# Performance work log

Measured on AMD Instinct MI355X. Metric: run time of the kernel, lower is better.

The kernel has to match this reference:

```python
import jax, jax.numpy as jnp
import numpy as np

NUM_USERS = 100000
NUM_ITEMS = 200000
N_NODES = NUM_USERS + NUM_ITEMS
LATENT_DIM = 64
N_LAYERS = 3
NNZ = 4000000


def setup_inputs() -> dict:
    key = jax.random.key(0)
    k1, k2, k3, k4, k5 = jax.random.split(key, 5)
    user_emb = 0.1 * jax.random.normal(k1, (NUM_USERS, LATENT_DIM), dtype=jnp.float32)
    item_emb = 0.1 * jax.random.normal(k2, (NUM_ITEMS, LATENT_DIM), dtype=jnp.float32)
    edge_rows = jax.random.randint(k3, (NNZ,), 0, N_NODES, dtype=jnp.int32)
    edge_cols = jax.random.randint(k4, (NNZ,), 0, N_NODES, dtype=jnp.int32)
    # normalized adjacency values (positive, small, like 1/sqrt(d_i d_j))
    edge_vals = jax.random.uniform(k5, (NNZ,), dtype=jnp.float32) * 0.1
    return {"user_emb": user_emb, "item_emb": item_emb,
            "edge_rows": edge_rows, "edge_cols": edge_cols, "edge_vals": edge_vals}


def _spmm(edge_rows, edge_cols, edge_vals, x, n):
    # sparse (COO) @ dense: gather source rows, scale, scatter-add to dest rows
    msg = edge_vals[:, None] * x[edge_cols]          # [nnz, D]
    return jax.ops.segment_sum(msg, edge_rows, num_segments=n)


def reference(user_emb, item_emb, edge_rows, edge_cols, edge_vals):
    n_users = user_emb.shape[0]
    n = n_users + item_emb.shape[0]
    all_emb = jnp.concatenate([user_emb, item_emb], axis=0)  # [N, D]
    embs = [all_emb]
    for _ in range(N_LAYERS):
        all_emb = _spmm(edge_rows, edge_cols, edge_vals, all_emb, n)
        embs.append(all_emb)
    light_out = jnp.mean(jnp.stack(embs, axis=1), axis=1)   # [N, D]
    users = light_out[:n_users]
    items = light_out[n_users:]
    return users, items
```

## Files before the change

kernel.cpp:

```cpp
#include <hip/hip_runtime.h>


#define N_USERS  100000
#define N_ITEMS  200000
#define N_NODES_ 300000
#define DIM      64
#define NNZ_     4000000
#define BSHIFT   10
#define NBUCKET  ((N_NODES_ + 1023) >> 10)
#define BCAP     14336
#define PA_CHUNK 4096
#define PA_BLOCKS ((NNZ_ + PA_CHUNK - 1) / PA_CHUNK)

typedef float        f32x4 __attribute__((ext_vector_type(4)));
typedef unsigned int u32x4 __attribute__((ext_vector_type(4)));
typedef int          i32x2 __attribute__((ext_vector_type(2)));
__device__ __forceinline__ float4 ntload_f4(const float4* p) {
    f32x4 v = __builtin_nontemporal_load((const f32x4*)p);
    return make_float4(v.x, v.y, v.z, v.w);
}
__device__ __forceinline__ uint4 ntload_u4(const uint4* p) {
    u32x4 v = __builtin_nontemporal_load((const u32x4*)p);
    return make_uint4(v.x, v.y, v.z, v.w);
}
__device__ __forceinline__ void ntstore_f4(float4* p, float4 x) {
    f32x4 v = {x.x, x.y, x.z, x.w};
    __builtin_nontemporal_store(v, (f32x4*)p);
}
__device__ __forceinline__ int2 ntload_i2(const int2* p) {
    i32x2 v = __builtin_nontemporal_load((const i32x2*)p);
    return make_int2(v.x, v.y);
}

__device__ __forceinline__ unsigned short f2bf(float f) {
    unsigned u = __float_as_uint(f);
    unsigned r = 0x7fffu + ((u >> 16) & 1u);
    return (unsigned short)((u + r) >> 16);
}
__device__ __forceinline__ void fma8(float* acc, float v, uint4 r) {
    acc[0] = fmaf(v, __uint_as_float(r.x << 16), acc[0]);
    acc[1] = fmaf(v, __uint_as_float(r.x & 0xffff0000u), acc[1]);
    acc[2] = fmaf(v, __uint_as_float(r.y << 16), acc[2]);
    acc[3] = fmaf(v, __uint_as_float(r.y & 0xffff0000u), acc[3]);
    acc[4] = fmaf(v, __uint_as_float(r.z << 16), acc[4]);
    acc[5] = fmaf(v, __uint_as_float(r.z & 0xffff0000u), acc[5]);
    acc[6] = fmaf(v, __uint_as_float(r.w << 16), acc[6]);
    acc[7] = fmaf(v, __uint_as_float(r.w & 0xffff0000u), acc[7]);
}
__device__ __forceinline__ uint4 pack8(const float* f) {
    unsigned a = (unsigned)f2bf(f[0]) | ((unsigned)f2bf(f[1]) << 16);
    unsigned b = (unsigned)f2bf(f[2]) | ((unsigned)f2bf(f[3]) << 16);
    unsigned c = (unsigned)f2bf(f[4]) | ((unsigned)f2bf(f[5]) << 16);
    unsigned d = (unsigned)f2bf(f[6]) | ((unsigned)f2bf(f[7]) << 16);
    return make_uint4(a, b, c, d);
}
__device__ __forceinline__ void unpack8(float* f, uint4 r) {
    f[0] = __uint_as_float(r.x << 16); f[1] = __uint_as_float(r.x & 0xffff0000u);
    f[2] = __uint_as_float(r.y << 16); f[3] = __uint_as_float(r.y & 0xffff0000u);
    f[4] = __uint_as_float(r.z << 16); f[5] = __uint_as_float(r.z & 0xffff0000u);
    f[6] = __uint_as_float(r.w << 16); f[7] = __uint_as_float(r.w & 0xffff0000u);
}

__global__ void init_bf(const float4* __restrict__ u, const float4* __restrict__ it,
                        uint4* __restrict__ Abf) {
    const int n_u = N_USERS * DIM / 8;
    const int n_t = N_NODES_ * DIM / 8;
    int i = blockIdx.x * blockDim.x + threadIdx.x;
    if (i >= n_t) return;
    float4 a, b;
    if (i < n_u) { a = u[2 * i];           b = u[2 * i + 1]; }
    else         { int j = i - n_u; a = it[2 * j]; b = it[2 * j + 1]; }
    float f[8] = {a.x, a.y, a.z, a.w, b.x, b.y, b.z, b.w};
    Abf[i] = pack8(f);
}

__global__ void gcur_init2(int* __restrict__ gcursor) {
    int t = threadIdx.x;
    if (t < NBUCKET) gcursor[t] = t * BCAP;
}

__global__ __launch_bounds__(256) void passA(const int* __restrict__ rows,
                                             const int* __restrict__ cols,
                                             const float* __restrict__ vals,
                                             int* __restrict__ gcursor,
                                             int2* __restrict__ binned) {
    __shared__ int  hist[NBUCKET];
    __shared__ int  base_l[NBUCKET];
    __shared__ int  gshift[NBUCKET];
    __shared__ int  sc[256];
    __shared__ int2 stage[PA_CHUNK];
    __shared__ unsigned short bIdA[PA_CHUNK];

    int tid = threadIdx.x;
    int base = blockIdx.x * PA_CHUNK;
    int cnt = NNZ_ - base; if (cnt > PA_CHUNK) cnt = PA_CHUNK;

    for (int i = tid; i < NBUCKET; i += 256) hist[i] = 0;
    __syncthreads();

    int rr[16], cc[16], vv[16];
    #pragma unroll
    for (int k = 0; k < 16; ++k) {
        int i = tid + (k << 8);
        if (i < cnt) {
            int e = base + i;
            rr[k] = rows[e];
            cc[k] = cols[e];
            vv[k] = __float_as_int(vals[e]);
            atomicAdd(&hist[rr[k] >> BSHIFT], 1);
        } else rr[k] = -1;
    }
    __syncthreads();

    int i0 = 2 * tid, i1 = 2 * tid + 1;
    int c0 = (i0 < NBUCKET) ? hist[i0] : 0;
    int c1 = (i1 < NBUCKET) ? hist[i1] : 0;
    sc[tid] = c0 + c1;
    __syncthreads();
    for (int off = 1; off < 256; off <<= 1) {
        int t = (tid >= off) ? sc[tid - off] : 0;
        __syncthreads();
        sc[tid] += t;
        __syncthreads();
    }
    int excl = (tid == 0) ? 0 : sc[tid - 1];
    if (i0 < NBUCKET) {
        base_l[i0] = excl;
        int g0 = c0 ? atomicAdd(&gcursor[i0], c0) : 0;
        gshift[i0] = g0 - excl;
        hist[i0] = 0;
    }
    if (i1 < NBUCKET) {
        base_l[i1] = excl + c0;
        int g1 = c1 ? atomicAdd(&gcursor[i1], c1) : 0;
        gshift[i1] = g1 - (excl + c0);
        hist[i1] = 0;
    }
    __syncthreads();

    #pragma unroll
    for (int k = 0; k < 16; ++k) {
        if (rr[k] >= 0) {
            int b = rr[k] >> BSHIFT;
            int kk = atomicAdd(&hist[b], 1);
            int pos = base_l[b] + kk;
            stage[pos] = make_int2(cc[k] | ((rr[k] & 1023) << 19), vv[k]);
            bIdA[pos] = (unsigned short)b;
        }
    }
    __syncthreads();

    #pragma unroll
    for (int k = 0; k < 16; ++k) {
        int i = tid + (k << 8);
        if (i < cnt) binned[gshift[bIdA[i]] + i] = stage[i];
    }
}

__global__ void bucket_scan(const int* __restrict__ gcursor,
                            int* __restrict__ bucket_base,
                            int* __restrict__ row_start) {
    __shared__ int lds[512];
    int t = threadIdx.x;
    int c = (t < NBUCKET) ? (gcursor[t] - t * BCAP) : 0;
    lds[t] = c;
    __syncthreads();
    for (int off = 1; off < 512; off <<= 1) {
        int v = (t >= off) ? lds[t - off] : 0;
        __syncthreads();
        lds[t] += v;
        __syncthreads();
    }
    if (t < NBUCKET) bucket_base[t] = lds[t] - c;
    if (t == 0) row_start[N_NODES_] = NNZ_;
}

__global__ __launch_bounds__(1024) void passB(const int* __restrict__ gcursor,
                                              const int* __restrict__ bucket_base,
                                              const int2* __restrict__ binned,
                                              int* __restrict__ row_start,
                                              int2* __restrict__ sedge) {
    __shared__ int lcnt[1024];
    __shared__ int wsum[16];
    int b = blockIdx.x;
    int t = threadIdx.x;
    int base = b * BCAP;
    int cnt = gcursor[b] - base;
    int csr0 = bucket_base[b];
    lcnt[t] = 0;
    __syncthreads();

    int lo[14], hv[14];
    #pragma unroll
    for (int k = 0; k < 14; ++k) {
        int i = t + (k << 10);
        if (i < cnt) {
            int2 p = ntload_i2(&binned[base + i]);
            lo[k] = p.x; hv[k] = p.y;
            atomicAdd(&lcnt[((unsigned)p.x >> 19) & 1023], 1);
        } else lo[k] = -1;
    }
    __syncthreads();

    int v = lcnt[t];
    int lane = t & 63;
    int wid = t >> 6;
    int sv = v;
    #pragma unroll
    for (int off = 1; off < 64; off <<= 1) {
        int tmp = __shfl_up(sv, off);
        if (lane >= off) sv += tmp;
    }
    if (lane == 63) wsum[wid] = sv;
    __syncthreads();
    if (t < 16) {
        int ws = wsum[t];
        #pragma unroll
        for (int off = 1; off < 16; off <<= 1) {
            int tmp = __shfl_up(ws, off);
            if (t >= off) ws += tmp;
        }
        wsum[t] = ws;
    }
    __syncthreads();
    int wbase = (wid == 0) ? 0 : wsum[wid - 1];
    int excl = wbase + sv - v;

    int gr = (b << BSHIFT) + t;
    if (gr < N_NODES_) row_start[gr] = csr0 + excl;
    lcnt[t] = excl;
    __syncthreads();

    #pragma unroll
    for (int k = 0; k < 14; ++k) {
        if (lo[k] >= 0) {
            int rl = ((unsigned)lo[k] >> 19) & 1023;
            int pos = atomicAdd(&lcnt[rl], 1);
            sedge[csr0 + pos] = make_int2(lo[k] & 0x7ffff, hv[k]);
        }
    }
}

template<bool FUSE>
__global__ __launch_bounds__(256) void spmm_bf_t(const int* __restrict__ row_start,
                                                 const int2* __restrict__ sedge,
                                                 const uint4* __restrict__ x,
                                                 uint4* __restrict__ y,
                                                 const float4* __restrict__ u,
                                                 const float4* __restrict__ it,
                                                 const uint4* __restrict__ x1,
                                                 const uint4* __restrict__ x2,
                                                 float4* __restrict__ out) {
    int w = blockIdx.x * 32 + (threadIdx.x >> 3);
    int d = threadIdx.x & 7;
    int s = row_start[w];
    int e = row_start[w + 1];
    float acc[8] = {0.f, 0.f, 0.f, 0.f, 0.f, 0.f, 0.f, 0.f};
    int i = s;
    for (; i + 1 < e; i += 2) {
        int2 p0 = sedge[i];
        int2 p1 = sedge[i + 1];
        uint4 r0 = x[((unsigned)p0.x << 3) + d];
        uint4 r1 = x[((unsigned)p1.x << 3) + d];
        fma8(acc, __int_as_float(p0.y), r0);
        fma8(acc, __int_as_float(p1.y), r1);
    }
    if (i < e) {
        int2 p0 = sedge[i];
        uint4 r0 = x[((unsigned)p0.x << 3) + d];
        fma8(acc, __int_as_float(p0.y), r0);
    }
    if (!FUSE) {
        y[(size_t)w * 8 + d] = pack8(acc);
    } else {
        const float4* src = (w < N_USERS) ? (u + (size_t)w * 16)
                                          : (it + (size_t)(w - N_USERS) * 16);
        float4 a  = ntload_f4(&src[2 * d]);
        float4 b2 = ntload_f4(&src[2 * d + 1]);
        float f0[8] = {a.x, a.y, a.z, a.w, b2.x, b2.y, b2.z, b2.w};
        float f1[8], f2[8];
        unpack8(f1, ntload_u4(&x1[(size_t)w * 8 + d]));
        unpack8(f2, x2[(size_t)w * 8 + d]);
        float o[8];
        #pragma unroll
        for (int k = 0; k < 8; ++k) o[k] = (f0[k] + f1[k] + f2[k] + acc[k]) * 0.25f;
        ntstore_f4(&out[(size_t)w * 16 + 2 * d],
                   make_float4(o[0], o[1], o[2], o[3]));
        ntstore_f4(&out[(size_t)w * 16 + 2 * d + 1],
                   make_float4(o[4], o[5], o[6], o[7]));
    }
}

extern "C" void kernel_launch(void* const* d_in, const int* in_sizes, int n_in,
                              void* d_out, int out_size, void* d_ws, size_t ws_size,
                              hipStream_t stream) {
    const float* user_emb = (const float*)d_in[0];
    const float* item_emb = (const float*)d_in[1];
    const int*   rows     = (const int*)d_in[2];
    const int*   cols     = (const int*)d_in[3];
    const float* vals     = (const float*)d_in[4];
    float* out = (float*)d_out;

    const size_t nE = (size_t)N_NODES_ * DIM;
    unsigned short* Abf = (unsigned short*)d_ws;
    unsigned short* Bbf = Abf + nE;
    unsigned short* Cbf = Bbf + nE;
    int* row_start   = (int*)(Cbf + nE);
    int* gcursor     = row_start + (N_NODES_ + 2);
    int* bucket_base = gcursor + 512;
    int2* binned = (int2*)(bucket_base + 512);
    int2* sedge  = binned + (size_t)NBUCKET * BCAP;

    const int n_t8 = (int)(nE / 8);
    const int ew_grid   = (n_t8 + 255) / 256;
    const int spmm_grid = N_NODES_ / 32;

    gcur_init2<<<1, 512, 0, stream>>>(gcursor);
    passA<<<PA_BLOCKS, 256, 0, stream>>>(rows, cols, vals, gcursor, binned);
    bucket_scan<<<1, 512, 0, stream>>>(gcursor, bucket_base, row_start);
    passB<<<NBUCKET, 1024, 0, stream>>>(gcursor, bucket_base, binned, row_start, sedge);

    init_bf<<<ew_grid, 256, 0, stream>>>((const float4*)user_emb, (const float4*)item_emb,
                                         (uint4*)Abf);
    spmm_bf_t<false><<<spmm_grid, 256, 0, stream>>>(row_start, sedge, (const uint4*)Abf,
                                                    (uint4*)Bbf, nullptr, nullptr,
                                                    nullptr, nullptr, nullptr);
    spmm_bf_t<false><<<spmm_grid, 256, 0, stream>>>(row_start, sedge, (const uint4*)Bbf,
                                                    (uint4*)Cbf, nullptr, nullptr,
                                                    nullptr, nullptr, nullptr);
    spmm_bf_t<true><<<spmm_grid, 256, 0, stream>>>(row_start, sedge, (const uint4*)Cbf,
                                                   nullptr,
                                                   (const float4*)user_emb,
                                                   (const float4*)item_emb,
                                                   (const uint4*)Bbf, (const uint4*)Cbf,
                                                   (float4*)out);
}
```

Baseline: 544.5 us.

## Fold bucket scan into passB, memset cursors, halve passA chunk, drop NT stores

```diff
diff --git a/kernel.cpp b/kernel.cpp
--- a/kernel.cpp
+++ b/kernel.cpp
@@ -9,7 +9,7 @@
 #define BSHIFT   10
 #define NBUCKET  ((N_NODES_ + 1023) >> 10)
 #define BCAP     14336
-#define PA_CHUNK 4096
+#define PA_CHUNK 2048
 #define PA_BLOCKS ((NNZ_ + PA_CHUNK - 1) / PA_CHUNK)
 
 typedef float        f32x4 __attribute__((ext_vector_type(4)));
@@ -22,10 +22,6 @@
 __device__ __forceinline__ uint4 ntload_u4(const uint4* p) {
     u32x4 v = __builtin_nontemporal_load((const u32x4*)p);
     return make_uint4(v.x, v.y, v.z, v.w);
-}
-__device__ __forceinline__ void ntstore_f4(float4* p, float4 x) {
-    f32x4 v = {x.x, x.y, x.z, x.w};
-    __builtin_nontemporal_store(v, (f32x4*)p);
 }
 __device__ __forceinline__ int2 ntload_i2(const int2* p) {
     i32x2 v = __builtin_nontemporal_load((const i32x2*)p);
@@ -74,11 +70,6 @@
     Abf[i] = pack8(f);
 }
 
-__global__ void gcur_init2(int* __restrict__ gcursor) {
-    int t = threadIdx.x;
-    if (t < NBUCKET) gcursor[t] = t * BCAP;
-}
-
 __global__ __launch_bounds__(256) void passA(const int* __restrict__ rows,
                                              const int* __restrict__ cols,
                                              const float* __restrict__ vals,
@@ -98,9 +89,9 @@
     for (int i = tid; i < NBUCKET; i += 256) hist[i] = 0;
     __syncthreads();
 
-    int rr[16], cc[16], vv[16];
-    #pragma unroll
-    for (int k = 0; k < 16; ++k) {
+    int rr[8], cc[8], vv[8];
+    #pragma unroll
+    for (int k = 0; k < 8; ++k) {
         int i = tid + (k << 8);
         if (i < cnt) {
             int e = base + i;
@@ -127,19 +118,19 @@
     if (i0 < NBUCKET) {
         base_l[i0] = excl;
         int g0 = c0 ? atomicAdd(&gcursor[i0], c0) : 0;
-        gshift[i0] = g0 - excl;
+        gshift[i0] = i0 * BCAP + g0 - excl;
         hist[i0] = 0;
     }
     if (i1 < NBUCKET) {
         base_l[i1] = excl + c0;
         int g1 = c1 ? atomicAdd(&gcursor[i1], c1) : 0;
-        gshift[i1] = g1 - (excl + c0);
+        gshift[i1] = i1 * BCAP + g1 - (excl + c0);
         hist[i1] = 0;
     }
     __syncthreads();
 
     #pragma unroll
-    for (int k = 0; k < 16; ++k) {
+    for (int k = 0; k < 8; ++k) {
         if (rr[k] >= 0) {
             int b = rr[k] >> BSHIFT;
             int kk = atomicAdd(&hist[b], 1);
@@ -151,44 +142,40 @@
     __syncthreads();
 
     #pragma unroll
-    for (int k = 0; k < 16; ++k) {
+    for (int k = 0; k < 8; ++k) {
         int i = tid + (k << 8);
         if (i < cnt) binned[gshift[bIdA[i]] + i] = stage[i];
     }
 }
 
-__global__ void bucket_scan(const int* __restrict__ gcursor,
-                            int* __restrict__ bucket_base,
-                            int* __restrict__ row_start) {
-    __shared__ int lds[512];
-    int t = threadIdx.x;
-    int c = (t < NBUCKET) ? (gcursor[t] - t * BCAP) : 0;
-    lds[t] = c;
-    __syncthreads();
-    for (int off = 1; off < 512; off <<= 1) {
-        int v = (t >= off) ? lds[t - off] : 0;
-        __syncthreads();
-        lds[t] += v;
-        __syncthreads();
-    }
-    if (t < NBUCKET) bucket_base[t] = lds[t] - c;
-    if (t == 0) row_start[N_NODES_] = NNZ_;
-}
-
 __global__ __launch_bounds__(1024) void passB(const int* __restrict__ gcursor,
-                                              const int* __restrict__ bucket_base,
                                               const int2* __restrict__ binned,
                                               int* __restrict__ row_start,
                                               int2* __restrict__ sedge) {
     __shared__ int lcnt[1024];
-    __shared__ int wsum[16];
+    __shared__ int wsum[17];
     int b = blockIdx.x;
     int t = threadIdx.x;
+    int lane = t & 63;
+    int wid = t >> 6;
     int base = b * BCAP;
-    int cnt = gcursor[b] - base;
-    int csr0 = bucket_base[b];
+    int cnt = gcursor[b];
+
+    int c = (t < b) ? gcursor[t] : 0;
+    #pragma unroll
+    for (int off = 1; off < 64; off <<= 1) c += __shfl_xor(c, off);
+    if (lane == 0) wsum[wid] = c;
+    __syncthreads();
+    if (t < 16) {
+        int s = wsum[t];
+        #pragma unroll
+        for (int off = 1; off < 16; off <<= 1) s += __shfl_xor(s, off);
+        if (t == 0) wsum[16] = s;
+    }
     lcnt[t] = 0;
     __syncthreads();
+    int csr0 = wsum[16];
+    if (b == NBUCKET - 1 && t == 0) row_start[N_NODES_] = NNZ_;
 
     int lo[14], hv[14];
     #pragma unroll
@@ -203,8 +190,6 @@
     __syncthreads();
 
     int v = lcnt[t];
-    int lane = t & 63;
-    int wid = t >> 6;
     int sv = v;
     #pragma unroll
     for (int off = 1; off < 64; off <<= 1) {
@@ -284,10 +269,8 @@
         float o[8];
         #pragma unroll
         for (int k = 0; k < 8; ++k) o[k] = (f0[k] + f1[k] + f2[k] + acc[k]) * 0.25f;
-        ntstore_f4(&out[(size_t)w * 16 + 2 * d],
-                   make_float4(o[0], o[1], o[2], o[3]));
-        ntstore_f4(&out[(size_t)w * 16 + 2 * d + 1],
-                   make_float4(o[4], o[5], o[6], o[7]));
+        out[(size_t)w * 16 + 2 * d]     = make_float4(o[0], o[1], o[2], o[3]);
+        out[(size_t)w * 16 + 2 * d + 1] = make_float4(o[4], o[5], o[6], o[7]);
     }
 }
 
@@ -307,18 +290,16 @@
     unsigned short* Cbf = Bbf + nE;
     int* row_start   = (int*)(Cbf + nE);
     int* gcursor     = row_start + (N_NODES_ + 2);
-    int* bucket_base = gcursor + 512;
-    int2* binned = (int2*)(bucket_base + 512);
+    int2* binned = (int2*)(gcursor + 512);
     int2* sedge  = binned + (size_t)NBUCKET * BCAP;
 
     const int n_t8 = (int)(nE / 8);
     const int ew_grid   = (n_t8 + 255) / 256;
     const int spmm_grid = N_NODES_ / 32;
 
-    gcur_init2<<<1, 512, 0, stream>>>(gcursor);
+    hipMemsetAsync(gcursor, 0, NBUCKET * sizeof(int), stream);
     passA<<<PA_BLOCKS, 256, 0, stream>>>(rows, cols, vals, gcursor, binned);
-    bucket_scan<<<1, 512, 0, stream>>>(gcursor, bucket_base, row_start);
-    passB<<<NBUCKET, 1024, 0, stream>>>(gcursor, bucket_base, binned, row_start, sedge);
+    passB<<<NBUCKET, 1024, 0, stream>>>(gcursor, binned, row_start, sedge);
 
     init_bf<<<ew_grid, 256, 0, stream>>>((const float4*)user_emb, (const float4*)item_emb,
                                          (uint4*)Abf);
```

After: 591.0 us. +8.5%, slower.
